# Performance work log

Hardware: AMD Instinct MI355X
Metric: run time of the kernel (lower is better)

Reference implementation:

```python
import jax, jax.numpy as jnp
import numpy as np

N, E = 40000, 640000
DIN, HID, H = 512, 128, 4
C = HID  # per-head channels; H*C == 512 == DIN
BN_EPS = 1e-5


def setup_inputs() -> dict:
    key = jax.random.key(0)
    ks = jax.random.split(key, 32)
    sc = 0.05
    d = {}
    d["x"] = jax.random.normal(ks[0], (N, DIN), jnp.float32)
    d["edge_index"] = jax.random.randint(ks[1], (2, E), 0, N)
    i = 2
    for l in (1, 2, 3):
        d[f"W{l}"] = jax.random.normal(ks[i], (DIN, H * C), jnp.float32) * sc; i += 1
        d[f"as{l}"] = jax.random.normal(ks[i], (H, C), jnp.float32) * sc; i += 1
        d[f"ad{l}"] = jax.random.normal(ks[i], (H, C), jnp.float32) * sc; i += 1
        d[f"b{l}"] = jnp.zeros((H * C,), jnp.float32)
        d[f"g{l}"] = jnp.ones((H * C,), jnp.float32)
        d[f"be{l}"] = jnp.zeros((H * C,), jnp.float32)
    d["Wg1"] = jax.random.normal(ks[i], (H * C, HID), jnp.float32) * sc; i += 1
    d["bg1"] = jnp.zeros((HID,), jnp.float32)
    d["Wg2"] = jax.random.normal(ks[i], (HID, 1), jnp.float32) * sc; i += 1
    d["bg2"] = jnp.zeros((1,), jnp.float32)
    d["Wf1"] = jax.random.normal(ks[i], (H * C, HID), jnp.float32) * sc; i += 1
    d["bf1"] = jnp.zeros((HID,), jnp.float32)
    d["Wf2"] = jax.random.normal(ks[i], (HID, HID), jnp.float32) * sc; i += 1
    d["bf2"] = jnp.zeros((HID,), jnp.float32)
    d["Wp"] = jax.random.normal(ks[i], (HID + H * C, HID), jnp.float32) * sc; i += 1
    d["bp"] = jnp.zeros((HID,), jnp.float32)
    return d


def _gat(x, src, dst, W, a_s, a_d, b):
    # PyG GATConv (concat=True, negative_slope=0.2, self-loops already in src/dst)
    n = x.shape[0]
    h = (x @ W).reshape(n, H, C)                      # [N,H,C]
    es = jnp.einsum('nhc,hc->nh', h, a_s)             # alpha_src per node
    ed = jnp.einsum('nhc,hc->nh', h, a_d)             # alpha_dst per node
    e = jax.nn.leaky_relu(es[src] + ed[dst], 0.2)     # [Etot,H]
    m = jax.ops.segment_max(e, dst, num_segments=n)   # softmax over incoming edges
    ex = jnp.exp(e - m[dst])
    s = jax.ops.segment_sum(ex, dst, num_segments=n)
    w = ex / (s[dst] + 1e-16)                         # [Etot,H]
    out = jax.ops.segment_sum(w[:, :, None] * h[src], dst, num_segments=n)
    return out.reshape(n, H * C) + b


def _bn(x, g, b):
    mu = x.mean(0)
    var = x.var(0)
    return (x - mu) * jax.lax.rsqrt(var + BN_EPS) * g + b


def reference(x, edge_index,
              W1, as1, ad1, b1, g1, be1,
              W2, as2, ad2, b2, g2, be2,
              W3, as3, ad3, b3, g3, be3,
              Wg1, bg1, Wg2, bg2, Wf1, bf1, Wf2, bf2, Wp, bp):
    n = x.shape[0]
    loops = jnp.arange(n)
    src = jnp.concatenate([edge_index[0], loops])
    dst = jnp.concatenate([edge_index[1], loops])

    h = jax.nn.leaky_relu(_bn(_gat(x, src, dst, W1, as1, ad1, b1), g1, be1), 0.2)
    h_res = h
    h = jax.nn.leaky_relu(_bn(_gat(h, src, dst, W2, as2, ad2, b2), g2, be2), 0.2) + h_res
    h_res = h
    h = jax.nn.leaky_relu(_bn(_gat(h, src, dst, W3, as3, ad3, b3), g3, be3), 0.2) + h_res

    attn_scores = (jnp.tanh(h @ Wg1 + bg1) @ Wg2 + bg2)[:, 0]   # [N]
    attn_w = jax.nn.softmax(attn_scores)                        # softmax over all nodes
    feat = jax.nn.relu(h @ Wf1 + bf1) @ Wf2 + bf2               # [N,HID]
    gated = (attn_w[:, None] * feat).sum(0)                     # [HID]
    global_pooled = h.mean(0, keepdims=True)                    # batch=None -> one graph
    combined = jnp.concatenate([gated[None, :], global_pooled], axis=-1)  # [1,640]
    out = (combined @ Wp + bp)[0]                               # [HID]
    return out, attn_scores
```

## Files before the change

kernel.cpp:

```cpp
#include <hip/hip_runtime.h>
#include <math.h>

#define N_NODES 40000
#define M_PAD   40064
#define N_EDGES 640000
#define ETOT    (N_EDGES + N_NODES)
#define DINC    512
#define NHEAD   4
#define CHD     128
#define BN_EPS  1e-5f

typedef __attribute__((ext_vector_type(8))) short bf16x8;
typedef __attribute__((ext_vector_type(4))) float f32x4;

static __device__ __forceinline__ float lrelu(float x) { return x > 0.f ? x : 0.2f * x; }

static __device__ __forceinline__ unsigned short f2b(float f) {
    union { float f; unsigned int u; } v; v.f = f;
    unsigned int r = (v.u + 0x7fff + ((v.u >> 16) & 1)) >> 16;
    return (unsigned short)r;
}
static __device__ __forceinline__ float b2f(unsigned short b) {
    union { unsigned int u; float f; } v; v.u = ((unsigned int)b) << 16;
    return v.f;
}
static __device__ __forceinline__ float lo16(unsigned int u) {
    union { unsigned int u; float f; } v; v.u = u << 16; return v.f;
}
static __device__ __forceinline__ float hi16(unsigned int u) {
    union { unsigned int u; float f; } v; v.u = u & 0xffff0000u; return v.f;
}

#define GLDS16(g, l) __builtin_amdgcn_global_load_lds( \
    (__attribute__((address_space(1))) void*)(g),      \
    (__attribute__((address_space(3))) void*)(l), 16, 0, 0)

__global__ void k_degree(const int* __restrict__ ei, int* __restrict__ cnt) {
    int e = blockIdx.x * 256 + threadIdx.x;
    if (e < ETOT) {
        int dst = (e < N_EDGES) ? ei[N_EDGES + e] : (e - N_EDGES);
        atomicAdd(&cnt[dst], 1);
    }
}

__global__ __launch_bounds__(64) void k_scan1(const int* __restrict__ deg, int* __restrict__ bsum) {
    int lane = threadIdx.x;
    int v = deg[blockIdx.x * 64 + lane];
#pragma unroll
    for (int off = 32; off; off >>= 1) v += __shfl_xor(v, off);
    if (lane == 0) bsum[blockIdx.x] = v;
}

__global__ __launch_bounds__(1024) void k_scan2(const int* __restrict__ bsum, int* __restrict__ bpref,
                                                int* __restrict__ rowptr) {
    __shared__ int buf[1024];
    int tid = threadIdx.x;
    int v = (tid < 625) ? bsum[tid] : 0;
    buf[tid] = v;
    __syncthreads();
    for (int off = 1; off < 1024; off <<= 1) {
        int t = (tid >= off) ? buf[tid - off] : 0;
        __syncthreads();
        buf[tid] += t;
        __syncthreads();
    }
    if (tid < 625) bpref[tid] = buf[tid] - v;
    if (tid == 0) rowptr[N_NODES] = ETOT;
}

__global__ __launch_bounds__(64) void k_scan3(const int* __restrict__ deg, const int* __restrict__ bpref,
                                              int* __restrict__ rowptr) {
    int lane = threadIdx.x;
    int i = blockIdx.x * 64 + lane;
    int v = deg[i];
    int inc = v;
#pragma unroll
    for (int off = 1; off < 64; off <<= 1) {
        int t = __shfl_up(inc, off);
        if (lane >= off) inc += t;
    }
    rowptr[i] = bpref[blockIdx.x] + inc - v;
}

__global__ void k_fill(const int* __restrict__ ei, const int* __restrict__ rowptr,
                       int* __restrict__ cnt, int* __restrict__ csr_src) {
    int e = blockIdx.x * 256 + threadIdx.x;
    if (e < ETOT) {
        int src, dst;
        if (e < N_EDGES) { src = ei[e]; dst = ei[N_EDGES + e]; }
        else             { src = e - N_EDGES; dst = src; }
        int pos = rowptr[dst] + atomicAdd(&cnt[dst], 1);
        csr_src[pos] = src;
    }
}

__global__ __launch_bounds__(256) void k_cvtx(const float4* __restrict__ xin, uint4* __restrict__ xb) {
    size_t i = (size_t)blockIdx.x * 256 + threadIdx.x;
    float4 a = xin[i * 2], b = xin[i * 2 + 1];
    uint4 o;
    o.x = (unsigned)f2b(a.x) | ((unsigned)f2b(a.y) << 16);
    o.y = (unsigned)f2b(a.z) | ((unsigned)f2b(a.w) << 16);
    o.z = (unsigned)f2b(b.x) | ((unsigned)f2b(b.y) << 16);
    o.w = (unsigned)f2b(b.z) | ((unsigned)f2b(b.w) << 16);
    xb[i] = o;
}

__global__ __launch_bounds__(256) void k_cvtw(const float* __restrict__ W, unsigned short* __restrict__ Wt,
                                              int K, int Nn) {
    int idx = blockIdx.x * 256 + threadIdx.x;
    int k = idx / Nn, n = idx % Nn;
    Wt[(size_t)n * K + k] = f2b(W[idx]);
}

template<int CBF16>
__global__ __launch_bounds__(256) void k_gemm_mfma(const unsigned short* __restrict__ A,
                                                   const unsigned short* __restrict__ Bt,
                                                   void* __restrict__ Cout,
                                                   int Nn, int K, int nbn) {
    __shared__ alignas(16) unsigned short As[128 * 64];
    __shared__ alignas(16) unsigned short Bs[128 * 64];
    const int tid  = threadIdx.x;
    const int wv   = tid >> 6;
    const int lane = tid & 63;
    const int bm = (blockIdx.x / nbn) * 128;
    const int bn = (blockIdx.x % nbn) * 128;
    const int wm = (wv >> 1) * 64;
    const int wn = (wv & 1) * 64;

    const int srow = lane >> 3;
    const int scol = (((lane & 7) ^ srow) * 8);
    const size_t a_base = (size_t)(bm + wv * 32 + srow) * K + scol;
    const size_t b_base = (size_t)(bn + wv * 32 + srow) * K + scol;

    f32x4 acc[4][4] = {};

    for (int k0 = 0; k0 < K; k0 += 64) {
#pragma unroll
        for (int q = 0; q < 4; ++q)
            GLDS16(A + a_base + (size_t)q * 8 * K + k0, &As[(wv * 32 + q * 8) * 64]);
#pragma unroll
        for (int q = 0; q < 4; ++q)
            GLDS16(Bt + b_base + (size_t)q * 8 * K + k0, &Bs[(wv * 32 + q * 8) * 64]);
        __syncthreads();

        const int r0 = lane & 15;
#pragma unroll
        for (int ks = 0; ks < 2; ++ks) {
            const int c = ks * 4 + (lane >> 4);
            bf16x8 af[4], bfr[4];
#pragma unroll
            for (int i = 0; i < 4; ++i) {
                int row = wm + i * 16 + r0;
                af[i] = *(const bf16x8*)&As[row * 64 + ((c ^ (row & 7)) * 8)];
            }
#pragma unroll
            for (int j = 0; j < 4; ++j) {
                int row = wn + j * 16 + r0;
                bfr[j] = *(const bf16x8*)&Bs[row * 64 + ((c ^ (row & 7)) * 8)];
            }
#pragma unroll
            for (int i = 0; i < 4; ++i)
#pragma unroll
                for (int j = 0; j < 4; ++j)
                    acc[i][j] = __builtin_amdgcn_mfma_f32_16x16x32_bf16(af[i], bfr[j], acc[i][j], 0, 0, 0);
        }
        __syncthreads();
    }

    const int crow0 = bm + wm + (lane >> 4) * 4;
    const int ccol  = bn + wn + (lane & 15);
#pragma unroll
    for (int i = 0; i < 4; ++i)
#pragma unroll
        for (int j = 0; j < 4; ++j)
#pragma unroll
            for (int r = 0; r < 4; ++r) {
                size_t off = (size_t)(crow0 + i * 16 + r) * Nn + ccol + j * 16;
                if (CBF16) ((unsigned short*)Cout)[off] = f2b(acc[i][j][r]);
                else       ((float*)Cout)[off] = acc[i][j][r];
            }
}

__global__ __launch_bounds__(256) void k_esed(const unsigned short* __restrict__ hb,
                                              const float* __restrict__ as_,
                                              const float* __restrict__ ad_,
                                              float* __restrict__ es,
                                              float* __restrict__ ed) {
    int n = blockIdx.x * 4 + (threadIdx.x >> 6);
    int lane = threadIdx.x & 63;
    int head = lane >> 4;
    uint4 hv = *(const uint4*)&hb[(size_t)n * DINC + lane * 8];
    const float* ap = as_ + head * CHD + (lane & 15) * 8;
    const float* dp = ad_ + head * CHD + (lane & 15) * 8;
    float4 a0 = *(const float4*)ap, a1 = *(const float4*)(ap + 4);
    float4 d0 = *(const float4*)dp, d1 = *(const float4*)(dp + 4);
    float h0 = lo16(hv.x), h1 = hi16(hv.x), h2 = lo16(hv.y), h3 = hi16(hv.y);
    float h4 = lo16(hv.z), h5 = hi16(hv.z), h6 = lo16(hv.w), h7 = hi16(hv.w);
    float s = h0 * a0.x + h1 * a0.y + h2 * a0.z + h3 * a0.w
            + h4 * a1.x + h5 * a1.y + h6 * a1.z + h7 * a1.w;
    float d = h0 * d0.x + h1 * d0.y + h2 * d0.z + h3 * d0.w
            + h4 * d1.x + h5 * d1.y + h6 * d1.z + h7 * d1.w;
#pragma unroll
    for (int off = 8; off; off >>= 1) {
        s += __shfl_xor(s, off);
        d += __shfl_xor(d, off);
    }
    if ((lane & 15) == 0) { es[n * NHEAD + head] = s; ed[n * NHEAD + head] = d; }
}

__global__ __launch_bounds__(256) void k_wts(const float4* __restrict__ es4,
                                             const float4* __restrict__ ed4,
                                             const int* __restrict__ rowptr,
                                             const int* __restrict__ csr_src,
                                             float4* __restrict__ wbuf4,
                                             float4* __restrict__ inv4) {
    int n = blockIdx.x * 4 + (threadIdx.x >> 6);
    int lane = threadIdx.x & 63;
    int start = rowptr[n], end = rowptr[n + 1];
    float4 edn = ed4[n];
    float4 mx = make_float4(-1e30f, -1e30f, -1e30f, -1e30f);
    for (int j0 = start; j0 < end; j0 += 64) {
        int j = j0 + lane;
        if (j < end) {
            int s = csr_src[j];
            float4 e = es4[s];
            mx.x = fmaxf(mx.x, lrelu(e.x + edn.x));
            mx.y = fmaxf(mx.y, lrelu(e.y + edn.y));
            mx.z = fmaxf(mx.z, lrelu(e.z + edn.z));
            mx.w = fmaxf(mx.w, lrelu(e.w + edn.w));
        }
    }
#pragma unroll
    for (int off = 32; off; off >>= 1) {
        mx.x = fmaxf(mx.x, __shfl_xor(mx.x, off));
        mx.y = fmaxf(mx.y, __shfl_xor(mx.y, off));
        mx.z = fmaxf(mx.z, __shfl_xor(mx.z, off));
        mx.w = fmaxf(mx.w, __shfl_xor(mx.w, off));
    }
    float4 sum = make_float4(0.f, 0.f, 0.f, 0.f);
    for (int j0 = start; j0 < end; j0 += 64) {
        int j = j0 + lane;
        if (j < end) {
            int s = csr_src[j];
            float4 e = es4[s];
            float4 ex;
            ex.x = expf(lrelu(e.x + edn.x) - mx.x);
            ex.y = expf(lrelu(e.y + edn.y) - mx.y);
            ex.z = expf(lrelu(e.z + edn.z) - mx.z);
            ex.w = expf(lrelu(e.w + edn.w) - mx.w);
            wbuf4[j] = ex;
            sum.x += ex.x; sum.y += ex.y; sum.z += ex.z; sum.w += ex.w;
        }
    }
#pragma unroll
    for (int off = 32; off; off >>= 1) {
        sum.x += __shfl_xor(sum.x, off);
        sum.y += __shfl_xor(sum.y, off);
        sum.z += __shfl_xor(sum.z, off);
        sum.w += __shfl_xor(sum.w, off);
    }
    if (lane == 0) {
        float4 iv;
        iv.x = 1.f / (sum.x + 1e-16f);
        iv.y = 1.f / (sum.y + 1e-16f);
        iv.z = 1.f / (sum.z + 1e-16f);
        iv.w = 1.f / (sum.w + 1e-16f);
        inv4[n] = iv;
    }
}

__global__ __launch_bounds__(256) void k_agg(const unsigned short* __restrict__ hb,
                                             const int* __restrict__ rowptr,
                                             const int* __restrict__ csr_src,
                                             const float* __restrict__ wbuf,
                                             const float* __restrict__ invp,
                                             unsigned short* __restrict__ aggb) {
    __shared__ float part[4][512];
    const int n = blockIdx.x;
    const int tid = threadIdx.x;
    const int grp = tid >> 6;
    const int lane = tid & 63;
    const int head = lane >> 4;
    const int start = rowptr[n], end = rowptr[n + 1];

    float acc[8] = {};
    int j = start + grp;
    int s_n = 0; float w_n = 0.f;
    if (j < end) { s_n = csr_src[j]; w_n = wbuf[j * 4 + head]; }
    while (j < end) {
        int s = s_n; float w = w_n;
        int j2 = j + 4;
        if (j2 < end) { s_n = csr_src[j2]; w_n = wbuf[j2 * 4 + head]; }
        uint4 hv = *(const uint4*)&hb[(size_t)s * DINC + lane * 8];
        acc[0] += w * lo16(hv.x); acc[1] += w * hi16(hv.x);
        acc[2] += w * lo16(hv.y); acc[3] += w * hi16(hv.y);
        acc[4] += w * lo16(hv.z); acc[5] += w * hi16(hv.z);
        acc[6] += w * lo16(hv.w); acc[7] += w * hi16(hv.w);
        j = j2;
    }
    *(float4*)&part[grp][lane * 8]     = make_float4(acc[0], acc[1], acc[2], acc[3]);
    *(float4*)&part[grp][lane * 8 + 4] = make_float4(acc[4], acc[5], acc[6], acc[7]);
    __syncthreads();
    const int c = tid * 2;
    float v0 = part[0][c] + part[1][c] + part[2][c] + part[3][c];
    float v1 = part[0][c + 1] + part[1][c + 1] + part[2][c + 1] + part[3][c + 1];
    float iv = invp[(n << 2) + (c >> 7)];
    v0 *= iv; v1 *= iv;
    unsigned int o = (unsigned)f2b(v0) | ((unsigned)f2b(v1) << 16);
    *(unsigned int*)&aggb[(size_t)n * DINC + c] = o;
}

__global__ __launch_bounds__(256) void k_bn_stats(const unsigned short* __restrict__ aggb,
                                                  float* __restrict__ stats) {
    int tid = threadIdx.x;
    int row0 = blockIdx.x * 64;
    int c0 = tid * 2;
    float s0 = 0, q0 = 0, s1 = 0, q1 = 0;
    for (int r = row0; r < row0 + 64; ++r) {
        unsigned int hv = *(const unsigned int*)&aggb[(size_t)r * DINC + c0];
        float v0 = lo16(hv), v1 = hi16(hv);
        s0 += v0; q0 += v0 * v0;
        s1 += v1; q1 += v1 * v1;
    }
    atomicAdd(&stats[c0], s0);
    atomicAdd(&stats[c0 + 1], s1);
    atomicAdd(&stats[DINC + c0], q0);
    atomicAdd(&stats[DINC + c0 + 1], q1);
}

__global__ __launch_bounds__(512) void k_bn_fin(const float* __restrict__ stats,
                                                const float* __restrict__ g,
                                                const float* __restrict__ be,
                                                float* __restrict__ ab) {
    int c = threadIdx.x;
    float mu = stats[c] * (1.f / N_NODES);
    float var = stats[DINC + c] * (1.f / N_NODES) - mu * mu;
    float rstd = rsqrtf(var + BN_EPS);
    float A = g[c] * rstd;
    ab[c] = A;
    ab[DINC + c] = be[c] - mu * A;
}

__global__ __launch_bounds__(256) void k_bn_act(const unsigned short* __restrict__ aggb,
                                                const float* __restrict__ ab,
                                                unsigned short* __restrict__ curb,
                                                int res) {
    size_t idx = (size_t)blockIdx.x * 256 + threadIdx.x;
    int c4 = ((int)(idx & 127)) * 4;
    ushort4 v = *(const ushort4*)&aggb[idx * 4];
    float4 A = *(const float4*)(ab + c4);
    float4 B = *(const float4*)(ab + DINC + c4);
    float x0 = lrelu(b2f(v.x) * A.x + B.x);
    float x1 = lrelu(b2f(v.y) * A.y + B.y);
    float x2 = lrelu(b2f(v.z) * A.z + B.z);
    float x3 = lrelu(b2f(v.w) * A.w + B.w);
    if (res) {
        ushort4 r = *(const ushort4*)&curb[idx * 4];
        x0 += b2f(r.x); x1 += b2f(r.y); x2 += b2f(r.z); x3 += b2f(r.w);
    }
    ushort4 o;
    o.x = f2b(x0); o.y = f2b(x1); o.z = f2b(x2); o.w = f2b(x3);
    *(ushort4*)&curb[idx * 4] = o;
}

__global__ __launch_bounds__(256) void k_scores(float* __restrict__ Gf,
                                                const float* __restrict__ bg1,
                                                const float* __restrict__ Wg2,
                                                const float* __restrict__ bg2,
                                                const float* __restrict__ bf1,
                                                float* __restrict__ scores) {
    int n = blockIdx.x * 4 + (threadIdx.x >> 6);
    int lane = threadIdx.x & 63;
    float acc = 0.f;
#pragma unroll
    for (int rep = 0; rep < 2; ++rep) {
        int j = lane + rep * 64;
        float t = tanhf(Gf[(size_t)n * 256 + j] + bg1[j]);
        acc += t * Wg2[j];
        float f = Gf[(size_t)n * 256 + 128 + j] + bf1[j];
        Gf[(size_t)n * 256 + 128 + j] = fmaxf(f, 0.f);
    }
#pragma unroll
    for (int off = 32; off; off >>= 1) acc += __shfl_xor(acc, off);
    if (lane == 0) scores[n] = acc + bg2[0];
}

__global__ __launch_bounds__(1024) void k_softmax(const float* __restrict__ scores, float* __restrict__ sm) {
    __shared__ float red[16];
    int tid = threadIdx.x, lane = tid & 63, wv = tid >> 6;
    float m = -1e30f;
    for (int i = tid; i < N_NODES; i += 1024) m = fmaxf(m, scores[i]);
#pragma unroll
    for (int off = 32; off; off >>= 1) m = fmaxf(m, __shfl_xor(m, off));
    if (lane == 0) red[wv] = m;
    __syncthreads();
    float mall = red[0];
    for (int i = 1; i < 16; ++i) mall = fmaxf(mall, red[i]);
    __syncthreads();
    float s = 0.f;
    for (int i = tid; i < N_NODES; i += 1024) s += expf(scores[i] - mall);
#pragma unroll
    for (int off = 32; off; off >>= 1) s += __shfl_xor(s, off);
    if (lane == 0) red[wv] = s;
    __syncthreads();
    if (tid == 0) {
        float tot = 0.f;
        for (int i = 0; i < 16; ++i) tot += red[i];
        sm[0] = mall; sm[1] = tot;
    }
}

__global__ __launch_bounds__(640) void k_vpool(const float* __restrict__ Gf,
                                               const unsigned short* __restrict__ hb,
                                               const float* __restrict__ scores,
                                               const float* __restrict__ sm,
                                               float* __restrict__ v,
                                               float* __restrict__ pooled) {
    int tid = threadIdx.x;
    int row0 = blockIdx.x * 64;
    float mall = sm[0];
    float invS = 1.f / sm[1];
    if (tid < 128) {
        float acc = 0.f;
        for (int r = row0; r < row0 + 64; ++r) {
            float w = expf(scores[r] - mall) * invS;
            acc += w * Gf[(size_t)r * 256 + 128 + tid];
        }
        atomicAdd(&v[tid], acc);
    } else {
        int c = tid - 128;
        float acc = 0.f;
        for (int r = row0; r < row0 + 64; ++r) acc += b2f(hb[(size_t)r * DINC + c]);
        atomicAdd(&pooled[c], acc * (1.f / N_NODES));
    }
}

__global__ __launch_bounds__(128) void k_final(const float* __restrict__ v,
                                               const float* __restrict__ pooled,
                                               const float* __restrict__ Wf2,
                                               const float* __restrict__ bf2,
                                               const float* __restrict__ Wp,
                                               const float* __restrict__ bp,
                                               float* __restrict__ out) {
    __shared__ float sg[128];
    int o = threadIdx.x;
    float g = bf2[o];
    for (int k = 0; k < 128; ++k) g += v[k] * Wf2[k * 128 + o];
    sg[o] = g;
    __syncthreads();
    float acc = bp[o];
    for (int c = 0; c < 128; ++c) acc += sg[c] * Wp[c * 128 + o];
    for (int j = 0; j < 512; ++j) acc += pooled[j] * Wp[(128 + j) * 128 + o];
    out[o] = acc;
}

extern "C" void kernel_launch(void* const* d_in, const int* in_sizes, int n_in,
                              void* d_out, int out_size, void* d_ws, size_t ws_size,
                              hipStream_t stream) {
    const float* x  = (const float*)d_in[0];
    const int*   ei = (const int*)d_in[1];
    const float* Wg1 = (const float*)d_in[20];
    const float* bg1 = (const float*)d_in[21];
    const float* Wg2 = (const float*)d_in[22];
    const float* bg2 = (const float*)d_in[23];
    const float* Wf1 = (const float*)d_in[24];
    const float* bf1 = (const float*)d_in[25];
    const float* Wf2 = (const float*)d_in[26];
    const float* bf2 = (const float*)d_in[27];
    const float* Wp  = (const float*)d_in[28];
    const float* bp  = (const float*)d_in[29];
    float* out = (float*)d_out;

    char* base = (char*)d_ws;
    size_t off = 0;
    auto take = [&](size_t nbytes) -> char* {
        char* p = base + off;
        off += (nbytes + 255) & ~(size_t)255;
        return p;
    };
    unsigned short* hb   = (unsigned short*)take((size_t)M_PAD * DINC * 2);
    unsigned short* curb = (unsigned short*)take((size_t)M_PAD * DINC * 2);
    unsigned short* xb   = (unsigned short*)take((size_t)M_PAD * DINC * 2);
    unsigned short* aggb = (unsigned short*)take((size_t)M_PAD * DINC * 2);
    float* Gf    = (float*)take((size_t)M_PAD * 256 * 4);
    float* es    = (float*)take((size_t)N_NODES * NHEAD * 4);
    float* ed    = (float*)take((size_t)N_NODES * NHEAD * 4);
    float* wbuf  = (float*)take((size_t)ETOT * NHEAD * 4);
    float* invp  = (float*)take((size_t)N_NODES * NHEAD * 4);
    int*   rowptr= (int*)take((size_t)(N_NODES + 1) * 4);
    int*   cnt   = (int*)take((size_t)N_NODES * 4);
    int*   csr   = (int*)take((size_t)ETOT * 4);
    int*   bsum  = (int*)take(625 * 4);
    int*   bpref = (int*)take(625 * 4);
    float* stats = (float*)take(DINC * 2 * 4);
    float* ab    = (float*)take(DINC * 2 * 4);
    float* sm    = (float*)take(2 * 4);
    float* vbuf  = (float*)take(128 * 4);
    float* pooled= (float*)take(DINC * 4);
    unsigned short* Wt1  = (unsigned short*)take((size_t)DINC * DINC * 2);
    unsigned short* Wt2  = (unsigned short*)take((size_t)DINC * DINC * 2);
    unsigned short* Wt3  = (unsigned short*)take((size_t)DINC * DINC * 2);
    unsigned short* Wct  = (unsigned short*)take((size_t)256 * DINC * 2);

    k_cvtx<<<(N_NODES * DINC / 8) / 256, 256, 0, stream>>>((const float4*)x, (uint4*)xb);
    hipMemsetAsync(xb + (size_t)N_NODES * DINC, 0, (size_t)(M_PAD - N_NODES) * DINC * 2, stream);
    hipMemsetAsync(curb + (size_t)N_NODES * DINC, 0, (size_t)(M_PAD - N_NODES) * DINC * 2, stream);
    k_cvtw<<<DINC * DINC / 256, 256, 0, stream>>>((const float*)d_in[2],  Wt1, DINC, DINC);
    k_cvtw<<<DINC * DINC / 256, 256, 0, stream>>>((const float*)d_in[8],  Wt2, DINC, DINC);
    k_cvtw<<<DINC * DINC / 256, 256, 0, stream>>>((const float*)d_in[14], Wt3, DINC, DINC);
    k_cvtw<<<DINC * 128 / 256, 256, 0, stream>>>(Wg1, Wct, DINC, 128);
    k_cvtw<<<DINC * 128 / 256, 256, 0, stream>>>(Wf1, Wct + (size_t)128 * DINC, DINC, 128);

    hipMemsetAsync(cnt, 0, N_NODES * 4, stream);
    k_degree<<<(ETOT + 255) / 256, 256, 0, stream>>>(ei, cnt);
    k_scan1<<<625, 64, 0, stream>>>(cnt, bsum);
    k_scan2<<<1, 1024, 0, stream>>>(bsum, bpref, rowptr);
    k_scan3<<<625, 64, 0, stream>>>(cnt, bpref, rowptr);
    hipMemsetAsync(cnt, 0, N_NODES * 4, stream);
    k_fill<<<(ETOT + 255) / 256, 256, 0, stream>>>(ei, rowptr, cnt, csr);

    const unsigned short* Wts[3] = {Wt1, Wt2, Wt3};
    const unsigned short* in = xb;
    for (int l = 0; l < 3; ++l) {
        const float* as_ = (const float*)d_in[2 + l * 6 + 1];
        const float* ad_ = (const float*)d_in[2 + l * 6 + 2];
        const float* g   = (const float*)d_in[2 + l * 6 + 4];
        const float* be  = (const float*)d_in[2 + l * 6 + 5];

        k_gemm_mfma<1><<<(M_PAD / 128) * (DINC / 128), 256, 0, stream>>>(in, Wts[l], hb, DINC, DINC, DINC / 128);
        k_esed<<<N_NODES / 4, 256, 0, stream>>>(hb, as_, ad_, es, ed);
        k_wts<<<N_NODES / 4, 256, 0, stream>>>((const float4*)es, (const float4*)ed, rowptr, csr,
                                               (float4*)wbuf, (float4*)invp);
        k_agg<<<N_NODES, 256, 0, stream>>>(hb, rowptr, csr, wbuf, invp, aggb);
        hipMemsetAsync(stats, 0, DINC * 2 * 4, stream);
        k_bn_stats<<<N_NODES / 64, 256, 0, stream>>>(aggb, stats);
        k_bn_fin<<<1, 512, 0, stream>>>(stats, g, be, ab);
        k_bn_act<<<(N_NODES * (DINC / 4)) / 256, 256, 0, stream>>>(aggb, ab, curb, l > 0 ? 1 : 0);
        in = curb;
    }

    k_gemm_mfma<0><<<(M_PAD / 128) * 2, 256, 0, stream>>>(curb, Wct, Gf, 256, DINC, 2);

    float* scores = out + 128;
    k_scores<<<N_NODES / 4, 256, 0, stream>>>(Gf, bg1, Wg2, bg2, bf1, scores);
    k_softmax<<<1, 1024, 0, stream>>>(scores, sm);
    hipMemsetAsync(vbuf, 0, 128 * 4, stream);
    hipMemsetAsync(pooled, 0, DINC * 4, stream);
    k_vpool<<<N_NODES / 64, 640, 0, stream>>>(Gf, curb, scores, sm, vbuf, pooled);
    k_final<<<1, 128, 0, stream>>>(vbuf, pooled, Wf2, bf2, Wp, bp, out);
}
```

Measured before the change: 903.0 us.

## Fuse attention logits into GEMM epilogue, one-wave-per-node aggregation, wider BN act

The per-node attention logits (es/ed) are now computed in the GEMM epilogue from the fp32 accumulators, using shuffles and LDS atomics. This removes the separate k_esed kernel and its re-read of h. The aggregation kernel now gives each wave one node with a 4-way unrolled gather, replacing the old block-per-node layout with an LDS reduction. The BN activation kernel processes 8 bf16 values per thread instead of 4. The es/ed buffers are enlarged to the padded row count so the padding rows can be written safely.

After: 925.8 us. 1.03x slower.

```diff
diff --git a/kernel.cpp b/kernel.cpp
--- a/kernel.cpp
+++ b/kernel.cpp
@@ -29,6 +29,13 @@
 }
 static __device__ __forceinline__ float hi16(unsigned int u) {
     union { unsigned int u; float f; } v; v.u = u & 0xffff0000u; return v.f;
+}
+
+static __device__ __forceinline__ void fma8(float* acc, uint4 hv, float wgt) {
+    acc[0] += wgt * lo16(hv.x); acc[1] += wgt * hi16(hv.x);
+    acc[2] += wgt * lo16(hv.y); acc[3] += wgt * hi16(hv.y);
+    acc[4] += wgt * lo16(hv.z); acc[5] += wgt * hi16(hv.z);
+    acc[6] += wgt * lo16(hv.w); acc[7] += wgt * hi16(hv.w);
 }
 
 #define GLDS16(g, l) __builtin_amdgcn_global_load_lds( \
@@ -112,11 +119,15 @@
     Wt[(size_t)n * K + k] = f2b(W[idx]);
 }
 
-template<int CBF16>
+template<int CBF16, int EPI>
 __global__ __launch_bounds__(256) void k_gemm_mfma(const unsigned short* __restrict__ A,
                                                    const unsigned short* __restrict__ Bt,
                                                    void* __restrict__ Cout,
-                                                   int Nn, int K, int nbn) {
+                                                   int Nn, int K, int nbn,
+                                                   const float* __restrict__ as_,
+                                                   const float* __restrict__ ad_,
+                                                   float* __restrict__ es,
+                                                   float* __restrict__ ed) {
     __shared__ alignas(16) unsigned short As[128 * 64];
     __shared__ alignas(16) unsigned short Bs[128 * 64];
     const int tid  = threadIdx.x;
@@ -179,33 +190,44 @@
                 if (CBF16) ((unsigned short*)Cout)[off] = f2b(acc[i][j][r]);
                 else       ((float*)Cout)[off] = acc[i][j][r];
             }
-}
-
-__global__ __launch_bounds__(256) void k_esed(const unsigned short* __restrict__ hb,
-                                              const float* __restrict__ as_,
-                                              const float* __restrict__ ad_,
-                                              float* __restrict__ es,
-                                              float* __restrict__ ed) {
-    int n = blockIdx.x * 4 + (threadIdx.x >> 6);
-    int lane = threadIdx.x & 63;
-    int head = lane >> 4;
-    uint4 hv = *(const uint4*)&hb[(size_t)n * DINC + lane * 8];
-    const float* ap = as_ + head * CHD + (lane & 15) * 8;
-    const float* dp = ad_ + head * CHD + (lane & 15) * 8;
-    float4 a0 = *(const float4*)ap, a1 = *(const float4*)(ap + 4);
-    float4 d0 = *(const float4*)dp, d1 = *(const float4*)(dp + 4);
-    float h0 = lo16(hv.x), h1 = hi16(hv.x), h2 = lo16(hv.y), h3 = hi16(hv.y);
-    float h4 = lo16(hv.z), h5 = hi16(hv.z), h6 = lo16(hv.w), h7 = hi16(hv.w);
-    float s = h0 * a0.x + h1 * a0.y + h2 * a0.z + h3 * a0.w
-            + h4 * a1.x + h5 * a1.y + h6 * a1.z + h7 * a1.w;
-    float d = h0 * d0.x + h1 * d0.y + h2 * d0.z + h3 * d0.w
-            + h4 * d1.x + h5 * d1.y + h6 * d1.z + h7 * d1.w;
-#pragma unroll
-    for (int off = 8; off; off >>= 1) {
-        s += __shfl_xor(s, off);
-        d += __shfl_xor(d, off);
-    }
-    if ((lane & 15) == 0) { es[n * NHEAD + head] = s; ed[n * NHEAD + head] = d; }
+
+    if (EPI) {
+        const int head = bn >> 7;
+        float asv[4], adv[4];
+#pragma unroll
+        for (int j = 0; j < 4; ++j) {
+            int cc = head * CHD + wn + j * 16 + (lane & 15);
+            asv[j] = as_[cc];
+            adv[j] = ad_[cc];
+        }
+        float* sE = (float*)As;
+        sE[tid] = 0.f;
+        __syncthreads();
+#pragma unroll
+        for (int i = 0; i < 4; ++i)
+#pragma unroll
+            for (int r = 0; r < 4; ++r) {
+                float e = acc[i][0][r] * asv[0] + acc[i][1][r] * asv[1]
+                        + acc[i][2][r] * asv[2] + acc[i][3][r] * asv[3];
+                float d = acc[i][0][r] * adv[0] + acc[i][1][r] * adv[1]
+                        + acc[i][2][r] * adv[2] + acc[i][3][r] * adv[3];
+#pragma unroll
+                for (int off = 8; off; off >>= 1) {
+                    e += __shfl_xor(e, off);
+                    d += __shfl_xor(d, off);
+                }
+                if ((lane & 15) == 0) {
+                    int rloc = wm + i * 16 + (lane >> 4) * 4 + r;
+                    atomicAdd(&sE[rloc], e);
+                    atomicAdd(&sE[128 + rloc], d);
+                }
+            }
+        __syncthreads();
+        if (tid < 128) {
+            es[(size_t)(bm + tid) * NHEAD + head] = sE[tid];
+            ed[(size_t)(bm + tid) * NHEAD + head] = sE[128 + tid];
+        }
+    }
 }
 
 __global__ __launch_bounds__(256) void k_wts(const float4* __restrict__ es4,
@@ -275,39 +297,38 @@
                                              const float* __restrict__ wbuf,
                                              const float* __restrict__ invp,
                                              unsigned short* __restrict__ aggb) {
-    __shared__ float part[4][512];
-    const int n = blockIdx.x;
-    const int tid = threadIdx.x;
-    const int grp = tid >> 6;
-    const int lane = tid & 63;
+    const int n = blockIdx.x * 4 + (threadIdx.x >> 6);
+    const int lane = threadIdx.x & 63;
     const int head = lane >> 4;
     const int start = rowptr[n], end = rowptr[n + 1];
 
     float acc[8] = {};
-    int j = start + grp;
-    int s_n = 0; float w_n = 0.f;
-    if (j < end) { s_n = csr_src[j]; w_n = wbuf[j * 4 + head]; }
-    while (j < end) {
-        int s = s_n; float w = w_n;
-        int j2 = j + 4;
-        if (j2 < end) { s_n = csr_src[j2]; w_n = wbuf[j2 * 4 + head]; }
+    int j = start;
+    for (; j + 3 < end; j += 4) {
+        int s0 = csr_src[j], s1 = csr_src[j + 1], s2 = csr_src[j + 2], s3 = csr_src[j + 3];
+        float w0 = wbuf[j * 4 + head];
+        float w1 = wbuf[(j + 1) * 4 + head];
+        float w2 = wbuf[(j + 2) * 4 + head];
+        float w3 = wbuf[(j + 3) * 4 + head];
+        uint4 h0 = *(const uint4*)&hb[(size_t)s0 * DINC + lane * 8];
+        uint4 h1 = *(const uint4*)&hb[(size_t)s1 * DINC + lane * 8];
+        uint4 h2 = *(const uint4*)&hb[(size_t)s2 * DINC + lane * 8];
+        uint4 h3 = *(const uint4*)&hb[(size_t)s3 * DINC + lane * 8];
+        fma8(acc, h0, w0); fma8(acc, h1, w1); fma8(acc, h2, w2); fma8(acc, h3, w3);
+    }
+    for (; j < end; ++j) {
+        int s = csr_src[j];
+        float wgt = wbuf[j * 4 + head];
         uint4 hv = *(const uint4*)&hb[(size_t)s * DINC + lane * 8];
-        acc[0] += w * lo16(hv.x); acc[1] += w * hi16(hv.x);
-        acc[2] += w * lo16(hv.y); acc[3] += w * hi16(hv.y);
-        acc[4] += w * lo16(hv.z); acc[5] += w * hi16(hv.z);
-        acc[6] += w * lo16(hv.w); acc[7] += w * hi16(hv.w);
-        j = j2;
-    }
-    *(float4*)&part[grp][lane * 8]     = make_float4(acc[0], acc[1], acc[2], acc[3]);
-    *(float4*)&part[grp][lane * 8 + 4] = make_float4(acc[4], acc[5], acc[6], acc[7]);
-    __syncthreads();
-    const int c = tid * 2;
-    float v0 = part[0][c] + part[1][c] + part[2][c] + part[3][c];
-    float v1 = part[0][c + 1] + part[1][c + 1] + part[2][c + 1] + part[3][c + 1];
-    float iv = invp[(n << 2) + (c >> 7)];
-    v0 *= iv; v1 *= iv;
-    unsigned int o = (unsigned)f2b(v0) | ((unsigned)f2b(v1) << 16);
-    *(unsigned int*)&aggb[(size_t)n * DINC + c] = o;
+        fma8(acc, hv, wgt);
+    }
+    float iv = invp[n * NHEAD + head];
+    uint4 o;
+    o.x = (unsigned)f2b(acc[0] * iv) | ((unsigned)f2b(acc[1] * iv) << 16);
+    o.y = (unsigned)f2b(acc[2] * iv) | ((unsigned)f2b(acc[3] * iv) << 16);
+    o.z = (unsigned)f2b(acc[4] * iv) | ((unsigned)f2b(acc[5] * iv) << 16);
+    o.w = (unsigned)f2b(acc[6] * iv) | ((unsigned)f2b(acc[7] * iv) << 16);
+    *(uint4*)&aggb[(size_t)n * DINC + lane * 8] = o;
 }
 
 __global__ __launch_bounds__(256) void k_bn_stats(const unsigned short* __restrict__ aggb,
@@ -346,21 +367,26 @@
                                                 unsigned short* __restrict__ curb,
                                                 int res) {
     size_t idx = (size_t)blockIdx.x * 256 + threadIdx.x;
-    int c4 = ((int)(idx & 127)) * 4;
-    ushort4 v = *(const ushort4*)&aggb[idx * 4];
-    float4 A = *(const float4*)(ab + c4);
-    float4 B = *(const float4*)(ab + DINC + c4);
-    float x0 = lrelu(b2f(v.x) * A.x + B.x);
-    float x1 = lrelu(b2f(v.y) * A.y + B.y);
-    float x2 = lrelu(b2f(v.z) * A.z + B.z);
-    float x3 = lrelu(b2f(v.w) * A.w + B.w);
+    int c8 = ((int)(idx & 63)) * 8;
+    uint4 v = *(const uint4*)&aggb[idx * 8];
+    float xv[8] = { lo16(v.x), hi16(v.x), lo16(v.y), hi16(v.y),
+                    lo16(v.z), hi16(v.z), lo16(v.w), hi16(v.w) };
+#pragma unroll
+    for (int q = 0; q < 8; ++q)
+        xv[q] = lrelu(xv[q] * ab[c8 + q] + ab[DINC + c8 + q]);
     if (res) {
-        ushort4 r = *(const ushort4*)&curb[idx * 4];
-        x0 += b2f(r.x); x1 += b2f(r.y); x2 += b2f(r.z); x3 += b2f(r.w);
-    }
-    ushort4 o;
-    o.x = f2b(x0); o.y = f2b(x1); o.z = f2b(x2); o.w = f2b(x3);
-    *(ushort4*)&curb[idx * 4] = o;
+        uint4 r = *(const uint4*)&curb[idx * 8];
+        xv[0] += lo16(r.x); xv[1] += hi16(r.x);
+        xv[2] += lo16(r.y); xv[3] += hi16(r.y);
+        xv[4] += lo16(r.z); xv[5] += hi16(r.z);
+        xv[6] += lo16(r.w); xv[7] += hi16(r.w);
+    }
+    uint4 o;
+    o.x = (unsigned)f2b(xv[0]) | ((unsigned)f2b(xv[1]) << 16);
+    o.y = (unsigned)f2b(xv[2]) | ((unsigned)f2b(xv[3]) << 16);
+    o.z = (unsigned)f2b(xv[4]) | ((unsigned)f2b(xv[5]) << 16);
+    o.w = (unsigned)f2b(xv[6]) | ((unsigned)f2b(xv[7]) << 16);
+    *(uint4*)&curb[idx * 8] = o;
 }
 
 __global__ __launch_bounds__(256) void k_scores(float* __restrict__ Gf,
@@ -483,8 +509,8 @@
     unsigned short* xb   = (unsigned short*)take((size_t)M_PAD * DINC * 2);
     unsigned short* aggb = (unsigned short*)take((size_t)M_PAD * DINC * 2);
     float* Gf    = (float*)take((size_t)M_PAD * 256 * 4);
-    float* es    = (float*)take((size_t)N_NODES * NHEAD * 4);
-    float* ed    = (float*)take((size_t)N_NODES * NHEAD * 4);
+    float* es    = (float*)take((size_t)M_PAD * NHEAD * 4);
+    float* ed    = (float*)take((size_t)M_PAD * NHEAD * 4);
     float* wbuf  = (float*)take((size_t)ETOT * NHEAD * 4);
     float* invp  = (float*)take((size_t)N_NODES * NHEAD * 4);
     int*   rowptr= (int*)take((size_t)(N_NODES + 1) * 4);
@@ -527,19 +553,20 @@
         const float* g   = (const float*)d_in[2 + l * 6 + 4];
         const float* be  = (const float*)d_in[2 + l * 6 + 5];
 
-        k_gemm_mfma<1><<<(M_PAD / 128) * (DINC / 128), 256, 0, stream>>>(in, Wts[l], hb, DINC, DINC, DINC / 128);
-        k_esed<<<N_NODES / 4, 256, 0, stream>>>(hb, as_, ad_, es, ed);
+        k_gemm_mfma<1, 1><<<(M_PAD / 128) * (DINC / 128), 256, 0, stream>>>(
+            in, Wts[l], hb, DINC, DINC, DINC / 128, as_, ad_, es, ed);
         k_wts<<<N_NODES / 4, 256, 0, stream>>>((const float4*)es, (const float4*)ed, rowptr, csr,
                                                (float4*)wbuf, (float4*)invp);
-        k_agg<<<N_NODES, 256, 0, stream>>>(hb, rowptr, csr, wbuf, invp, aggb);
+        k_agg<<<N_NODES / 4, 256, 0, stream>>>(hb, rowptr, csr, wbuf, invp, aggb);
         hipMemsetAsync(stats, 0, DINC * 2 * 4, stream);
         k_bn_stats<<<N_NODES / 64, 256, 0, stream>>>(aggb, stats);
         k_bn_fin<<<1, 512, 0, stream>>>(stats, g, be, ab);
-        k_bn_act<<<(N_NODES * (DINC / 4)) / 256, 256, 0, stream>>>(aggb, ab, curb, l > 0 ? 1 : 0);
+        k_bn_act<<<(N_NODES * (DINC / 8)) / 256, 256, 0, stream>>>(aggb, ab, curb, l > 0 ? 1 : 0);
         in = curb;
     }
 
-    k_gemm_mfma<0><<<(M_PAD / 128) * 2, 256, 0, stream>>>(curb, Wct, Gf, 256, DINC, 2);
+    k_gemm_mfma<0, 0><<<(M_PAD / 128) * 2, 256, 0, stream>>>(
+        curb, Wct, Gf, 256, DINC, 2, nullptr, nullptr, nullptr, nullptr);
 
     float* scores = out + 128;
     k_scores<<<N_NODES / 4, 256, 0, stream>>>(Gf, bg1, Wg2, bg2, bf1, scores);
```
